# Kernel tuning notes

Measured on AMD Instinct MI355X. Metric: run time of the kernel, lower is better.

## Reference

```python
import jax, jax.numpy as jnp
import numpy as np

B, S, D = 4, 2048, 512
H, HD = 8, 64  # head_num, head_dim


def setup_inputs() -> dict:
    key = jax.random.key(0)
    ks = jax.random.split(key, 5)
    scale = 1.0 / np.sqrt(D)  # roughly xavier-scale
    return {
        "x": jax.random.normal(ks[0], (B, S, D), dtype=jnp.float32),
        "Wq": jax.random.normal(ks[1], (D, D), dtype=jnp.float32) * scale,
        "bq": jnp.zeros((D,), dtype=jnp.float32),
        "Wk": jax.random.normal(ks[2], (D, D), dtype=jnp.float32) * scale,
        "bk": jnp.zeros((D,), dtype=jnp.float32),
        "Wv": jax.random.normal(ks[3], (D, D), dtype=jnp.float32) * scale,
        "bv": jnp.zeros((D,), dtype=jnp.float32),
        "Wo": jax.random.normal(ks[4], (D, D), dtype=jnp.float32) * scale,
        "bo": jnp.zeros((D,), dtype=jnp.float32),
    }


def reference(x, Wq, bq, Wk, bk, Wv, bv, Wo, bo):
    b, s, _ = x.shape
    # torch Linear: y = x @ W.T + b; reshape to (b, heads, s, head_dim)
    def proj(W, bias):
        return (x @ W.T + bias).reshape(b, s, H, HD).transpose(0, 2, 1, 3)
    Q, K, V = proj(Wq, bq), proj(Wk, bk), proj(Wv, bv)
    inv_sqrt_dk = 1.0 / jnp.sqrt(jnp.float32(HD))
    scores = jnp.einsum("bhqd,bhkd->bhqk", Q, K) * inv_sqrt_dk
    attn = jax.nn.softmax(scores, axis=-1)  # F.softmax default -> last dim
    ctx = jnp.einsum("bhqk,bhkd->bhqd", attn, V)
    ctx = ctx.transpose(0, 2, 1, 3).reshape(b, s, D)
    return ctx @ Wo.T + bo
```

## Files before the change

### kernel.cpp

```cpp
#include <hip/hip_runtime.h>
#include <hip/hip_bf16.h>
#include <cstdint>
#include <cstddef>

#define S_LEN 2048
#define D_DIM 512
#define NHEAD 8
#define HDIM  64

typedef __attribute__((ext_vector_type(8)))  __bf16 b8;
typedef __attribute__((ext_vector_type(4)))  __bf16 b4;
typedef __attribute__((ext_vector_type(4)))  float  f4;
typedef __attribute__((ext_vector_type(16))) float  f16v;
typedef __attribute__((ext_vector_type(4)))  unsigned int u32x4;

#define AS_GLOBAL __attribute__((address_space(1)))
#define AS_LDS    __attribute__((address_space(3)))

__device__ __forceinline__ void load_lds16(const void* g, void* l) {
  __builtin_amdgcn_global_load_lds((const AS_GLOBAL void*)g, (AS_LDS void*)l, 16, 0, 0);
}

__device__ __forceinline__ f4 mfma16(b8 a, b8 b, f4 c) {
  return __builtin_amdgcn_mfma_f32_16x16x32_bf16(a, b, c, 0, 0, 0);
}
__device__ __forceinline__ f16v mfma32(b8 a, b8 b, f16v c) {
  return __builtin_amdgcn_mfma_f32_32x32x16_bf16(a, b, c, 0, 0, 0);
}

__device__ __forceinline__ float exp2v(float x) {
#if __has_builtin(__builtin_amdgcn_exp2f)
  return __builtin_amdgcn_exp2f(x);
#else
  float r; asm("v_exp_f32 %0, %1" : "=v"(r) : "v"(x)); return r;
#endif
}

__device__ __forceinline__ unsigned int pkbf(float lo, float hi_) {
  unsigned int r;
  asm("v_cvt_pk_bf16_f32 %0, %1, %2" : "=v"(r) : "v"(lo), "v"(hi_));
  return r;
}

__device__ __forceinline__ b8 lds_frag(const __bf16* base, int row, int bc) {
  return *reinterpret_cast<const b8*>((const char*)base + row * 128 + (bc ^ ((row & 7) << 4)));
}

__global__ __launch_bounds__(256) void cvt_kernel(const float* __restrict__ in,
                                                  __bf16* __restrict__ out) {
  int i = (blockIdx.x * 256 + threadIdx.x) * 4;
  float4 v = *reinterpret_cast<const float4*>(in + i);
  b4 o;
  o.x = (__bf16)v.x; o.y = (__bf16)v.y; o.z = (__bf16)v.z; o.w = (__bf16)v.w;
  *reinterpret_cast<b4*>(out + i) = o;
}

__global__ __launch_bounds__(256) void cvt_w_kernel(const float* __restrict__ w0, const float* __restrict__ w1,
                                                    const float* __restrict__ w2, const float* __restrict__ w3,
                                                    __bf16* o0, __bf16* o1, __bf16* o2, __bf16* o3) {
  const float* in = blockIdx.y == 0 ? w0 : blockIdx.y == 1 ? w1 : blockIdx.y == 2 ? w2 : w3;
  __bf16* out     = blockIdx.y == 0 ? o0 : blockIdx.y == 1 ? o1 : blockIdx.y == 2 ? o2 : o3;
  int i = (blockIdx.x * 256 + threadIdx.x) * 4;
  float4 v = *reinterpret_cast<const float4*>(in + i);
  b4 o;
  o.x = (__bf16)v.x; o.y = (__bf16)v.y; o.z = (__bf16)v.z; o.w = (__bf16)v.w;
  *reinterpret_cast<b4*>(out + i) = o;
}

__device__ __forceinline__ void gemm_core(const __bf16* __restrict__ A, const __bf16* __restrict__ W,
                                          int m0, int n0, __bf16* As, __bf16* Bs, f4 acc[4][4]) {
  const int t = threadIdx.x;
  const int lane = t & 63;
  const int w = t >> 6, wr = w >> 1, wc = w & 1;
  const f4 zero = {0.f, 0.f, 0.f, 0.f};
  #pragma unroll
  for (int mi = 0; mi < 4; ++mi)
    #pragma unroll
    for (int ni = 0; ni < 4; ++ni) acc[mi][ni] = zero;

  const char* Ab = (const char*)A;
  const char* Wb = (const char*)W;
  for (int kt = 0; kt < 512; kt += 64) {
    __syncthreads();
    #pragma unroll
    for (int i = 0; i < 4; ++i) {
      int o = i * 4096 + t * 16;
      int row = o >> 7, cb = o & 127;
      int scb = cb ^ ((row & 7) << 4);
      load_lds16(Ab + ((size_t)(m0 + row) * 512 + kt) * 2 + scb, (char*)As + o);
      load_lds16(Wb + ((size_t)(n0 + row) * 512 + kt) * 2 + scb, (char*)Bs + o);
    }
    __syncthreads();
    #pragma unroll
    for (int kk = 0; kk < 2; ++kk) {
      b8 af[4], bf[4];
      #pragma unroll
      for (int mi = 0; mi < 4; ++mi)
        af[mi] = lds_frag(As, wr * 64 + mi * 16 + (lane & 15), kk * 64 + ((lane >> 4) << 4));
      #pragma unroll
      for (int ni = 0; ni < 4; ++ni)
        bf[ni] = lds_frag(Bs, wc * 64 + ni * 16 + (lane & 15), kk * 64 + ((lane >> 4) << 4));
      #pragma unroll
      for (int mi = 0; mi < 4; ++mi)
        #pragma unroll
        for (int ni = 0; ni < 4; ++ni)
          acc[mi][ni] = mfma16(af[mi], bf[ni], acc[mi][ni]);
    }
  }
}

__global__ __launch_bounds__(256) void gemm_qkv_kernel(
    const __bf16* __restrict__ xb,
    const __bf16* __restrict__ wq, const __bf16* __restrict__ wk, const __bf16* __restrict__ wv,
    const float* __restrict__ bq, const float* __restrict__ bk, const float* __restrict__ bv,
    __bf16* Qo, __bf16* Ko, __bf16* Vo) {
  __shared__ __bf16 As[128 * 64];
  __shared__ __bf16 Bs[128 * 64];
  int z = blockIdx.z;
  const __bf16* W = z == 0 ? wq : (z == 1 ? wk : wv);
  const float* bias = z == 0 ? bq : (z == 1 ? bk : bv);
  __bf16* out = z == 0 ? Qo : (z == 1 ? Ko : Vo);
  const float sc = (z == 0) ? 0.18033688011112042f : 1.0f;
  int m0 = blockIdx.x * 128, n0 = blockIdx.y * 128;
  f4 acc[4][4];
  gemm_core(xb, W, m0, n0, As, Bs, acc);
  int t = threadIdx.x, lane = t & 63, w = t >> 6, wr = w >> 1, wc = w & 1;
  #pragma unroll
  for (int mi = 0; mi < 4; ++mi)
    #pragma unroll
    for (int ni = 0; ni < 4; ++ni)
      #pragma unroll
      for (int r = 0; r < 4; ++r) {
        int m = m0 + wr * 64 + mi * 16 + ((lane >> 4) << 2) + r;
        int n = n0 + wc * 64 + ni * 16 + (lane & 15);
        float v = (acc[mi][ni][r] + bias[n]) * sc;
        int b = m >> 11, s = m & 2047, h = n >> 6, hd = n & 63;
        out[(((size_t)(b * NHEAD + h)) * S_LEN + s) * HDIM + hd] = (__bf16)v;
      }
}

__global__ __launch_bounds__(256) void gemm_o_kernel(const __bf16* __restrict__ ctx,
                                                     const __bf16* __restrict__ wo,
                                                     const float* __restrict__ bo,
                                                     float* __restrict__ out) {
  __shared__ __bf16 As[128 * 64];
  __shared__ __bf16 Bs[128 * 64];
  int m0 = blockIdx.x * 128, n0 = blockIdx.y * 128;
  f4 acc[4][4];
  gemm_core(ctx, wo, m0, n0, As, Bs, acc);
  int t = threadIdx.x, lane = t & 63, w = t >> 6, wr = w >> 1, wc = w & 1;
  #pragma unroll
  for (int mi = 0; mi < 4; ++mi)
    #pragma unroll
    for (int ni = 0; ni < 4; ++ni)
      #pragma unroll
      for (int r = 0; r < 4; ++r) {
        int m = m0 + wr * 64 + mi * 16 + ((lane >> 4) << 2) + r;
        int n = n0 + wc * 64 + ni * 16 + (lane & 15);
        out[(size_t)m * D_DIM + n] = acc[mi][ni][r] + bo[n];
      }
}

__global__ __launch_bounds__(256) void transpose_v_kernel(const __bf16* __restrict__ V,
                                                          __bf16* __restrict__ Vt) {
  __shared__ __bf16 tile[64][72];
  int bh = blockIdx.y, s0 = blockIdx.x * 64;
  const __bf16* Vp = V + (size_t)bh * S_LEN * HDIM;
  __bf16* Vtp = Vt + (size_t)bh * HDIM * S_LEN;
  int t = threadIdx.x;
  #pragma unroll
  for (int i = 0; i < 4; ++i) {
    int q = t + i * 256;
    int row = q >> 4, c4 = (q & 15) * 4;
    b4 v = *reinterpret_cast<const b4*>(&Vp[(size_t)(s0 + row) * HDIM + c4]);
    *reinterpret_cast<b4*>(&tile[row][c4]) = v;
  }
  __syncthreads();
  #pragma unroll
  for (int i = 0; i < 4; ++i) {
    int q = t + i * 256;
    int d = q >> 4, s4 = (q & 15) * 4;
    b4 v;
    v.x = tile[s4 + 0][d]; v.y = tile[s4 + 1][d];
    v.z = tile[s4 + 2][d]; v.w = tile[s4 + 3][d];
    *reinterpret_cast<b4*>(&Vtp[(size_t)d * S_LEN + s0 + s4]) = v;
  }
}

#define NTG 16

#define MKFRAG(dst, st, base) do {                                   \
    unsigned int A0_ = pkbf((st)[(base)+0], (st)[(base)+1]);         \
    unsigned int A1_ = pkbf((st)[(base)+2], (st)[(base)+3]);         \
    unsigned int B0_ = pkbf((st)[(base)+4], (st)[(base)+5]);         \
    unsigned int B1_ = pkbf((st)[(base)+6], (st)[(base)+7]);         \
    asm("v_permlane32_swap_b32 %0, %1" : "+v"(A0_), "+v"(B0_));      \
    asm("v_permlane32_swap_b32 %0, %1" : "+v"(A1_), "+v"(B1_));      \
    u32x4 wv_; wv_.x = A0_; wv_.y = A1_; wv_.z = B0_; wv_.w = B1_;   \
    dst = __builtin_bit_cast(b8, wv_);                               \
  } while (0)

__global__ __launch_bounds__(512, 4) void attn_kernel(const __bf16* __restrict__ Q,
                                                      const __bf16* __restrict__ K,
                                                      const __bf16* __restrict__ Vt,
                                                      __bf16* __restrict__ ctx) {
  __shared__ __bf16 Ks[2][2][64 * 64];
  __shared__ __bf16 Vs[2][2][64 * 64];
  int t = threadIdx.x, lane = t & 63, w = t >> 6;
  int lane31 = lane & 31, hi = lane >> 5;
  int grp = w >> 2, qs = w & 3, t256 = t & 255;
  int bh = blockIdx.y, b = bh >> 3, h = bh & 7;
  int q = blockIdx.x * 128 + qs * 32 + lane31;
  const __bf16* Qp = Q + (size_t)bh * S_LEN * HDIM;
  const __bf16* Kp = K + (size_t)bh * S_LEN * HDIM;
  const __bf16* Vp = Vt + (size_t)bh * HDIM * S_LEN;
  const int kv0 = grp * (S_LEN / 2);

  b8 qf[4];
  #pragma unroll
  for (int ks = 0; ks < 4; ++ks)
    qf[ks] = *reinterpret_cast<const b8*>(&Qp[(size_t)q * HDIM + ks * 16 + hi * 8]);

  b8 ones;
  { u32x4 ov; ov.x = ov.y = ov.z = ov.w = 0x3F803F80u; ones = __builtin_bit_cast(b8, ov); }

  int foff[8];
  #pragma unroll
  for (int half = 0; half < 2; ++half)
    #pragma unroll
    for (int ks = 0; ks < 4; ++ks) {
      int row = half * 32 + lane31;
      int bc = hi * 16 + ks * 32;
      foff[half * 4 + ks] = row * 128 + (bc ^ ((row & 7) << 4));
    }

  int oA = t256 * 16, oB = 4096 + t256 * 16;
  int rA = oA >> 7, rB = oB >> 7;
  int sA = (oA & 127) ^ ((rA & 7) << 4), sB = (oB & 127) ^ ((rB & 7) << 4);
  const char* KgA = (const char*)Kp + (size_t)(kv0 + rA) * 128 + sA;
  const char* KgB = (const char*)Kp + (size_t)(kv0 + rB) * 128 + sB;
  const char* VgA = (const char*)Vp + (size_t)rA * (S_LEN * 2) + (size_t)kv0 * 2 + sA;
  const char* VgB = (const char*)Vp + (size_t)rB * (S_LEN * 2) + (size_t)kv0 * 2 + sB;
  char* KsB_ = (char*)&Ks[grp][0][0];
  char* VsB_ = (char*)&Vs[grp][0][0];

  const f16v Z16 = {0,0,0,0,0,0,0,0,0,0,0,0,0,0,0,0};
  f16v o0 = Z16, o1 = Z16;
  f16v sums = Z16;
  float mr = -1e30f;

  auto stage = [&](int buf) {
    load_lds16(KgA, KsB_ + buf * 8192 + oA);
    load_lds16(KgB, KsB_ + buf * 8192 + oB);
    load_lds16(VgA, VsB_ + buf * 8192 + oA);
    load_lds16(VgB, VsB_ + buf * 8192 + oB);
    KgA += 8192; KgB += 8192; VgA += 128; VgB += 128;
  };

  stage(0);
  __syncthreads();
  int cur = 0;

  for (int it = 0; it < NTG; ++it) {
    if (it + 1 < NTG) stage(cur ^ 1);

    const char* KsT = KsB_ + cur * 8192;
    const char* VsT = VsB_ + cur * 8192;

    f16v t0 = Z16, t1 = Z16;
    __builtin_amdgcn_s_setprio(1);
    #pragma unroll
    for (int ks = 0; ks < 4; ++ks) {
      b8 kf0 = *reinterpret_cast<const b8*>(KsT + foff[ks]);
      b8 kf1 = *reinterpret_cast<const b8*>(KsT + foff[4 + ks]);
      t0 = mfma32(kf0, qf[ks], t0);
      t1 = mfma32(kf1, qf[ks], t1);
    }
    __builtin_amdgcn_s_setprio(0);

    float a0 = fmaxf(fmaxf(t0[0], t0[8]),  fmaxf(t1[0], t1[8]));
    float a1 = fmaxf(fmaxf(t0[1], t0[9]),  fmaxf(t1[1], t1[9]));
    float a2 = fmaxf(fmaxf(t0[2], t0[10]), fmaxf(t1[2], t1[10]));
    float a3 = fmaxf(fmaxf(t0[3], t0[11]), fmaxf(t1[3], t1[11]));
    float a4 = fmaxf(fmaxf(t0[4], t0[12]), fmaxf(t1[4], t1[12]));
    float a5 = fmaxf(fmaxf(t0[5], t0[13]), fmaxf(t1[5], t1[13]));
    float a6 = fmaxf(fmaxf(t0[6], t0[14]), fmaxf(t1[6], t1[14]));
    float a7 = fmaxf(fmaxf(t0[7], t0[15]), fmaxf(t1[7], t1[15]));
    float mx = fmaxf(fmaxf(fmaxf(a0, a1), fmaxf(a2, a3)),
                     fmaxf(fmaxf(a4, a5), fmaxf(a6, a7)));
    mx = fmaxf(mx, __shfl_xor(mx, 32));

    if (!__all(mx - mr <= 11.5f)) {
      float mn = fmaxf(mr, mx);
      float al = exp2v(mr - mn);
      mr = mn;
      sums[0] *= al;
      o0 *= al;
      o1 *= al;
    }

    #pragma unroll
    for (int r = 0; r < 16; ++r) t0[r] = exp2v(t0[r] - mr);
    #pragma unroll
    for (int r = 0; r < 16; ++r) t1[r] = exp2v(t1[r] - mr);

    b8 pa[4];
    MKFRAG(pa[0], t0, 0);
    MKFRAG(pa[1], t0, 8);
    MKFRAG(pa[2], t1, 0);
    MKFRAG(pa[3], t1, 8);

    __builtin_amdgcn_s_setprio(1);
    #pragma unroll
    for (int ks = 0; ks < 4; ++ks) {
      b8 vf0 = *reinterpret_cast<const b8*>(VsT + foff[ks]);
      b8 vf1 = *reinterpret_cast<const b8*>(VsT + foff[4 + ks]);
      o0 = mfma32(vf0, pa[ks], o0);
      o1 = mfma32(vf1, pa[ks], o1);
      sums = mfma32(ones, pa[ks], sums);
    }
    __builtin_amdgcn_s_setprio(0);

    __syncthreads();
    cur ^= 1;
  }

  float l_own = sums[0];
  float* OL = (float*)&Ks[0][0][0];
  float* ML = OL + 8192;
  if (grp == 1) {
    #pragma unroll
    for (int g = 0; g < 4; ++g)
      #pragma unroll
      for (int j = 0; j < 4; ++j) {
        int d = 8 * g + 4 * hi + j;
        OL[(qs * 64 + d) * 32 + lane31]      = o0[4 * g + j];
        OL[(qs * 64 + 32 + d) * 32 + lane31] = o1[4 * g + j];
      }
    if (hi == 0) { ML[qs * 32 + lane31] = mr; ML[128 + qs * 32 + lane31] = l_own; }
  }
  __syncthreads();
  if (grp == 0) {
    float m1 = ML[qs * 32 + lane31], l1 = ML[128 + qs * 32 + lane31];
    float mm = fmaxf(mr, m1);
    float s0 = exp2v(mr - mm), s1 = exp2v(m1 - mm);
    float inv = 1.0f / (l_own * s0 + l1 * s1);
    __bf16* cp = ctx + (size_t)b * S_LEN * D_DIM + (size_t)q * D_DIM + (size_t)h * HDIM;
    #pragma unroll
    for (int g = 0; g < 4; ++g) {
      b4 v0, v1;
      #pragma unroll
      for (int j = 0; j < 4; ++j) {
        int d = 8 * g + 4 * hi + j;
        v0[j] = (__bf16)((o0[4 * g + j] * s0 + OL[(qs * 64 + d) * 32 + lane31] * s1) * inv);
        v1[j] = (__bf16)((o1[4 * g + j] * s0 + OL[(qs * 64 + 32 + d) * 32 + lane31] * s1) * inv);
      }
      int d0 = 8 * g + 4 * hi;
      *reinterpret_cast<b4*>(cp + d0)      = v0;
      *reinterpret_cast<b4*>(cp + 32 + d0) = v1;
    }
  }
}

extern "C" void kernel_launch(void* const* d_in, const int* in_sizes, int n_in,
                              void* d_out, int out_size, void* d_ws, size_t ws_size,
                              hipStream_t stream) {
  const float* x  = (const float*)d_in[0];
  const float* Wq = (const float*)d_in[1];
  const float* bq = (const float*)d_in[2];
  const float* Wk = (const float*)d_in[3];
  const float* bk = (const float*)d_in[4];
  const float* Wv = (const float*)d_in[5];
  const float* bv = (const float*)d_in[6];
  const float* Wo = (const float*)d_in[7];
  const float* bo = (const float*)d_in[8];
  float* out = (float*)d_out;

  char* ws = (char*)d_ws;
  __bf16* xb   = (__bf16*)(ws);
  __bf16* wqb  = xb  + 4194304;
  __bf16* wkb  = wqb + 262144;
  __bf16* wvb  = wkb + 262144;
  __bf16* wob  = wvb + 262144;
  __bf16* Qb   = wob + 262144;
  __bf16* Kb   = Qb  + 4194304;
  __bf16* Vb   = Kb  + 4194304;
  __bf16* Vtb  = Vb  + 4194304;
  __bf16* ctxb = xb;

  cvt_kernel<<<dim3(4096), dim3(256), 0, stream>>>(x, xb);
  cvt_w_kernel<<<dim3(256, 4), dim3(256), 0, stream>>>(Wq, Wk, Wv, Wo, wqb, wkb, wvb, wob);
  gemm_qkv_kernel<<<dim3(64, 4, 3), dim3(256), 0, stream>>>(xb, wqb, wkb, wvb, bq, bk, bv, Qb, Kb, Vb);
  transpose_v_kernel<<<dim3(32, 32), dim3(256), 0, stream>>>(Vb, Vtb);
  attn_kernel<<<dim3(16, 32), dim3(512), 0, stream>>>(Qb, Kb, Vtb, ctxb);
  gemm_o_kernel<<<dim3(64, 4), dim3(256), 0, stream>>>(ctxb, wob, bo, out);
}
```

Baseline: 108.2 us.

## Unroll attention loop by two, interleave P-fragment build with PV MFMAs, remap blocks

Unrolls the KV loop into two explicit buffer phases so LDS offsets become compile-time constants in a single flat shared array, and addresses LDS through explicit address-space pointers. The P fragments are now built one at a time inside the PV MFMA loop, which shortens register live ranges and lets the permlane work overlap the matrix ops. It also switches to a 1D grid with a block remap that spreads consecutive block IDs across heads, which likely targets cache or XCD locality. The cost is a larger code body and a block-to-tile mapping that depends on the grid size.

```diff
diff --git a/kernel.cpp b/kernel.cpp
--- a/kernel.cpp
+++ b/kernel.cpp
@@ -200,17 +200,68 @@
     dst = __builtin_bit_cast(b8, wv_);                               \
   } while (0)
 
+#define TILE(KO, VO) do {                                                     \
+    f16v t0 = Z16, t1 = Z16;                                                  \
+    __builtin_amdgcn_s_setprio(1);                                            \
+    _Pragma("unroll")                                                         \
+    for (int ks = 0; ks < 4; ++ks) {                                          \
+      b8 kf0 = *reinterpret_cast<const AS_LDS b8*>(sb + koff[ks] + (KO));     \
+      b8 kf1 = *reinterpret_cast<const AS_LDS b8*>(sb + koff[ks] + (KO) + 4096); \
+      t0 = mfma32(kf0, qf[ks], t0);                                           \
+      t1 = mfma32(kf1, qf[ks], t1);                                           \
+    }                                                                         \
+    __builtin_amdgcn_s_setprio(0);                                            \
+    float a0 = fmaxf(fmaxf(t0[0], t0[8]),  fmaxf(t1[0], t1[8]));              \
+    float a1 = fmaxf(fmaxf(t0[1], t0[9]),  fmaxf(t1[1], t1[9]));              \
+    float a2 = fmaxf(fmaxf(t0[2], t0[10]), fmaxf(t1[2], t1[10]));             \
+    float a3 = fmaxf(fmaxf(t0[3], t0[11]), fmaxf(t1[3], t1[11]));             \
+    float a4 = fmaxf(fmaxf(t0[4], t0[12]), fmaxf(t1[4], t1[12]));             \
+    float a5 = fmaxf(fmaxf(t0[5], t0[13]), fmaxf(t1[5], t1[13]));             \
+    float a6 = fmaxf(fmaxf(t0[6], t0[14]), fmaxf(t1[6], t1[14]));             \
+    float a7 = fmaxf(fmaxf(t0[7], t0[15]), fmaxf(t1[7], t1[15]));             \
+    float mx = fmaxf(fmaxf(fmaxf(a0, a1), fmaxf(a2, a3)),                     \
+                     fmaxf(fmaxf(a4, a5), fmaxf(a6, a7)));                    \
+    mx = fmaxf(mx, __shfl_xor(mx, 32));                                       \
+    if (!__all(mx - mr <= 11.5f)) {                                           \
+      float mn = fmaxf(mr, mx);                                               \
+      float al = exp2v(mr - mn);                                              \
+      mr = mn; sums[0] *= al; o0 *= al; o1 *= al;                             \
+    }                                                                         \
+    _Pragma("unroll")                                                         \
+    for (int r = 0; r < 16; ++r) t0[r] = exp2v(t0[r] - mr);                   \
+    _Pragma("unroll")                                                         \
+    for (int r = 0; r < 16; ++r) t1[r] = exp2v(t1[r] - mr);                   \
+    __builtin_amdgcn_s_setprio(1);                                            \
+    _Pragma("unroll")                                                         \
+    for (int ks = 0; ks < 4; ++ks) {                                          \
+      b8 pa;                                                                  \
+      if (ks == 0)      MKFRAG(pa, t0, 0);                                    \
+      else if (ks == 1) MKFRAG(pa, t0, 8);                                    \
+      else if (ks == 2) MKFRAG(pa, t1, 0);                                    \
+      else              MKFRAG(pa, t1, 8);                                    \
+      b8 vf0 = *reinterpret_cast<const AS_LDS b8*>(sb + koff[ks] + (VO));     \
+      b8 vf1 = *reinterpret_cast<const AS_LDS b8*>(sb + koff[ks] + (VO) + 4096); \
+      o0 = mfma32(vf0, pa, o0);                                               \
+      o1 = mfma32(vf1, pa, o1);                                               \
+      sums = mfma32(ones, pa, sums);                                          \
+    }                                                                         \
+    __builtin_amdgcn_s_setprio(0);                                            \
+  } while (0)
+
 __global__ __launch_bounds__(512, 4) void attn_kernel(const __bf16* __restrict__ Q,
                                                       const __bf16* __restrict__ K,
                                                       const __bf16* __restrict__ Vt,
                                                       __bf16* __restrict__ ctx) {
-  __shared__ __bf16 Ks[2][2][64 * 64];
-  __shared__ __bf16 Vs[2][2][64 * 64];
+  __shared__ char smem_[65536];
   int t = threadIdx.x, lane = t & 63, w = t >> 6;
   int lane31 = lane & 31, hi = lane >> 5;
   int grp = w >> 2, qs = w & 3, t256 = t & 255;
-  int bh = blockIdx.y, b = bh >> 3, h = bh & 7;
-  int q = blockIdx.x * 128 + qs * 32 + lane31;
+
+  int bid = blockIdx.x;
+  int nid = (bid & 7) * 64 + (bid >> 3);
+  int bh = nid >> 4, qtile = nid & 15;
+  int b = bh >> 3, h = bh & 7;
+  int q = qtile * 128 + qs * 32 + lane31;
   const __bf16* Qp = Q + (size_t)bh * S_LEN * HDIM;
   const __bf16* Kp = K + (size_t)bh * S_LEN * HDIM;
   const __bf16* Vp = Vt + (size_t)bh * HDIM * S_LEN;
@@ -224,15 +275,13 @@
   b8 ones;
   { u32x4 ov; ov.x = ov.y = ov.z = ov.w = 0x3F803F80u; ones = __builtin_bit_cast(b8, ov); }
 
-  int foff[8];
-  #pragma unroll
-  for (int half = 0; half < 2; ++half)
-    #pragma unroll
-    for (int ks = 0; ks < 4; ++ks) {
-      int row = half * 32 + lane31;
-      int bc = hi * 16 + ks * 32;
-      foff[half * 4 + ks] = row * 128 + (bc ^ ((row & 7) << 4));
-    }
+  const AS_LDS char* sb = (const AS_LDS char*)smem_;
+  unsigned koff[4];
+  #pragma unroll
+  for (int ks = 0; ks < 4; ++ks) {
+    int bc = hi * 16 + ks * 32;
+    koff[ks] = grp * 16384 + lane31 * 128 + (bc ^ ((lane31 & 7) << 4));
+  }
 
   int oA = t256 * 16, oB = 4096 + t256 * 16;
   int rA = oA >> 7, rB = oB >> 7;
@@ -241,8 +290,6 @@
   const char* KgB = (const char*)Kp + (size_t)(kv0 + rB) * 128 + sB;
   const char* VgA = (const char*)Vp + (size_t)rA * (S_LEN * 2) + (size_t)kv0 * 2 + sA;
   const char* VgB = (const char*)Vp + (size_t)rB * (S_LEN * 2) + (size_t)kv0 * 2 + sB;
-  char* KsB_ = (char*)&Ks[grp][0][0];
-  char* VsB_ = (char*)&Vs[grp][0][0];
 
   const f16v Z16 = {0,0,0,0,0,0,0,0,0,0,0,0,0,0,0,0};
   f16v o0 = Z16, o1 = Z16;
@@ -250,83 +297,29 @@
   float mr = -1e30f;
 
   auto stage = [&](int buf) {
-    load_lds16(KgA, KsB_ + buf * 8192 + oA);
-    load_lds16(KgB, KsB_ + buf * 8192 + oB);
-    load_lds16(VgA, VsB_ + buf * 8192 + oA);
-    load_lds16(VgB, VsB_ + buf * 8192 + oB);
+    char* ldsK = smem_ + grp * 16384 + buf * 8192;
+    load_lds16(KgA, ldsK + oA);
+    load_lds16(KgB, ldsK + oB);
+    load_lds16(VgA, ldsK + 32768 + oA);
+    load_lds16(VgB, ldsK + 32768 + oB);
     KgA += 8192; KgB += 8192; VgA += 128; VgB += 128;
   };
 
   stage(0);
   __syncthreads();
-  int cur = 0;
-
-  for (int it = 0; it < NTG; ++it) {
-    if (it + 1 < NTG) stage(cur ^ 1);
-
-    const char* KsT = KsB_ + cur * 8192;
-    const char* VsT = VsB_ + cur * 8192;
-
-    f16v t0 = Z16, t1 = Z16;
-    __builtin_amdgcn_s_setprio(1);
-    #pragma unroll
-    for (int ks = 0; ks < 4; ++ks) {
-      b8 kf0 = *reinterpret_cast<const b8*>(KsT + foff[ks]);
-      b8 kf1 = *reinterpret_cast<const b8*>(KsT + foff[4 + ks]);
-      t0 = mfma32(kf0, qf[ks], t0);
-      t1 = mfma32(kf1, qf[ks], t1);
-    }
-    __builtin_amdgcn_s_setprio(0);
-
-    float a0 = fmaxf(fmaxf(t0[0], t0[8]),  fmaxf(t1[0], t1[8]));
-    float a1 = fmaxf(fmaxf(t0[1], t0[9]),  fmaxf(t1[1], t1[9]));
-    float a2 = fmaxf(fmaxf(t0[2], t0[10]), fmaxf(t1[2], t1[10]));
-    float a3 = fmaxf(fmaxf(t0[3], t0[11]), fmaxf(t1[3], t1[11]));
-    float a4 = fmaxf(fmaxf(t0[4], t0[12]), fmaxf(t1[4], t1[12]));
-    float a5 = fmaxf(fmaxf(t0[5], t0[13]), fmaxf(t1[5], t1[13]));
-    float a6 = fmaxf(fmaxf(t0[6], t0[14]), fmaxf(t1[6], t1[14]));
-    float a7 = fmaxf(fmaxf(t0[7], t0[15]), fmaxf(t1[7], t1[15]));
-    float mx = fmaxf(fmaxf(fmaxf(a0, a1), fmaxf(a2, a3)),
-                     fmaxf(fmaxf(a4, a5), fmaxf(a6, a7)));
-    mx = fmaxf(mx, __shfl_xor(mx, 32));
-
-    if (!__all(mx - mr <= 11.5f)) {
-      float mn = fmaxf(mr, mx);
-      float al = exp2v(mr - mn);
-      mr = mn;
-      sums[0] *= al;
-      o0 *= al;
-      o1 *= al;
-    }
-
-    #pragma unroll
-    for (int r = 0; r < 16; ++r) t0[r] = exp2v(t0[r] - mr);
-    #pragma unroll
-    for (int r = 0; r < 16; ++r) t1[r] = exp2v(t1[r] - mr);
-
-    b8 pa[4];
-    MKFRAG(pa[0], t0, 0);
-    MKFRAG(pa[1], t0, 8);
-    MKFRAG(pa[2], t1, 0);
-    MKFRAG(pa[3], t1, 8);
-
-    __builtin_amdgcn_s_setprio(1);
-    #pragma unroll
-    for (int ks = 0; ks < 4; ++ks) {
-      b8 vf0 = *reinterpret_cast<const b8*>(VsT + foff[ks]);
-      b8 vf1 = *reinterpret_cast<const b8*>(VsT + foff[4 + ks]);
-      o0 = mfma32(vf0, pa[ks], o0);
-      o1 = mfma32(vf1, pa[ks], o1);
-      sums = mfma32(ones, pa[ks], sums);
-    }
-    __builtin_amdgcn_s_setprio(0);
-
+
+  #pragma unroll 1
+  for (int it2 = 0; it2 < NTG / 2; ++it2) {
+    stage(1);
+    TILE(0, 32768);
     __syncthreads();
-    cur ^= 1;
+    if (it2 < NTG / 2 - 1) stage(0);
+    TILE(8192, 40960);
+    __syncthreads();
   }
 
   float l_own = sums[0];
-  float* OL = (float*)&Ks[0][0][0];
+  float* OL = (float*)smem_;
   float* ML = OL + 8192;
   if (grp == 1) {
     #pragma unroll
@@ -392,6 +385,6 @@
   cvt_w_kernel<<<dim3(256, 4), dim3(256), 0, stream>>>(Wq, Wk, Wv, Wo, wqb, wkb, wvb, wob);
   gemm_qkv_kernel<<<dim3(64, 4, 3), dim3(256), 0, stream>>>(xb, wqb, wkb, wvb, bq, bk, bv, Qb, Kb, Vb);
   transpose_v_kernel<<<dim3(32, 32), dim3(256), 0, stream>>>(Vb, Vtb);
-  attn_kernel<<<dim3(16, 32), dim3(512), 0, stream>>>(Qb, Kb, Vtb, ctxb);
+  attn_kernel<<<dim3(512), dim3(512), 0, stream>>>(Qb, Kb, Vtb, ctxb);
   gemm_o_kernel<<<dim3(64, 4), dim3(256), 0, stream>>>(ctxb, wob, bo, out);
 }
```

Result: faster. 105.9 us (-2.1%).
